# Kernel tuning notes

Measured on AMD Instinct MI355X. Metric: run time of the kernel, lower is better.

The kernel has to match this reference:

```python
import jax, jax.numpy as jnp
import numpy as np

RES = 128
STEPSIZE = 0.5
NEAR, FAR, BG = 0.2, 3.0, 1.0
ALPHA_INIT = 0.01
XYZ_MIN, XYZ_MAX = -1.0, 1.0
N_RAYS = 1024
RGB_LATENT = 15
MULTIRES = 6
EMB_DIM = 3 + 3 * 2 * MULTIRES  # 39
DIM0 = RGB_LATENT + EMB_DIM     # 54
VOXEL = (XYZ_MAX - XYZ_MIN) / RES  # ((2^3)/RES^3)^(1/3)
N_SAMPLES = int(np.linalg.norm(np.array([RES] * 3) * 2 + 1) / STEPSIZE) + 1  # 891
ACT_SHIFT = float(np.log(1.0 / (1.0 - ALPHA_INIT) - 1.0))


def embed_dirs(d):
    # NeRF positional encoding, include_inputs=True, multires=6 -> 39 dims
    freqs = 2.0 ** jnp.arange(MULTIRES, dtype=d.dtype)
    ang = d[..., None, :] * freqs[:, None]  # [M,6,3]
    return jnp.concatenate([d, jnp.sin(ang).reshape(d.shape[0], -1), jnp.cos(ang).reshape(d.shape[0], -1)], -1)


def grid_sample3d(g, coords):
    # g: [C,D,H,W]; coords: [M,3] in (-1,1), torch grid_sample convention
    # (comp0 -> W axis, comp1 -> H axis, comp2 -> D axis), align_corners=True,
    # border-clamped indices (sampled out-of-box points are masked out anyway).
    C, D, H, W = g.shape
    x = (coords[:, 0] + 1) * 0.5 * (W - 1)
    y = (coords[:, 1] + 1) * 0.5 * (H - 1)
    z = (coords[:, 2] + 1) * 0.5 * (D - 1)
    x0, y0, z0 = jnp.floor(x), jnp.floor(y), jnp.floor(z)
    fx, fy, fz = x - x0, y - y0, z - z0
    x0i = jnp.clip(x0.astype(jnp.int32), 0, W - 1); x1i = jnp.clip(x0i + 1, 0, W - 1)
    y0i = jnp.clip(y0.astype(jnp.int32), 0, H - 1); y1i = jnp.clip(y0i + 1, 0, H - 1)
    z0i = jnp.clip(z0.astype(jnp.int32), 0, D - 1); z1i = jnp.clip(z0i + 1, 0, D - 1)
    gf = g.reshape(C, -1)
    def gv(zi, yi, xi):
        return gf[:, (zi * H + yi) * W + xi]  # [C,M]
    c = (((gv(z0i, y0i, x0i) * (1 - fx) + gv(z0i, y0i, x1i) * fx) * (1 - fy)
          + (gv(z0i, y1i, x0i) * (1 - fx) + gv(z0i, y1i, x1i) * fx) * fy) * (1 - fz)
         + ((gv(z1i, y0i, x0i) * (1 - fx) + gv(z1i, y0i, x1i) * fx) * (1 - fy)
            + (gv(z1i, y1i, x0i) * (1 - fx) + gv(z1i, y1i, x1i) * fx) * fy) * fz)
    return c.T  # [M,C]


def _forward(rays_o, rays_d, viewdirs, grid, sobel_kernel, w0, b0, w1, b1, w2, b2, w3, b3):
    # --- sample_ray: ray/AABB intersection + uniform stepping ---
    vec = jnp.where(rays_d == 0, 1e-6, rays_d)
    rate_a = (XYZ_MAX - rays_o) / vec
    rate_b = (XYZ_MIN - rays_o) / vec
    t_min = jnp.clip(jnp.minimum(rate_a, rate_b).max(-1), NEAR, FAR)
    t_max = jnp.clip(jnp.maximum(rate_a, rate_b).min(-1), NEAR, FAR)
    mask_ray = t_max <= t_min
    rng = jnp.arange(N_SAMPLES, dtype=rays_o.dtype)[None]
    step = STEPSIZE * VOXEL * rng
    interpx = t_min[:, None] + step / jnp.linalg.norm(rays_d, axis=-1, keepdims=True)
    pts = rays_o[:, None, :] + rays_d[:, None, :] * interpx[..., None]  # [N,S,3]
    inbox = (~mask_ray[:, None]) & (~((pts < XYZ_MIN) | (pts > XYZ_MAX)).any(-1))
    mflat = inbox.reshape(-1)

    # --- sobel normals grid (GridReg.forward(calc_normals=True)) ---
    density_grid = grid[None, :1]  # [1,1,D,H,W]
    nrm = jax.lax.conv_general_dilated(density_grid, sobel_kernel, (1, 1, 1), [(2, 2)] * 3,
                                       dimension_numbers=('NCDHW', 'OIDHW', 'NCDHW'))  # [1,3,D,H,W]
    nrm = -nrm / jnp.maximum(jnp.linalg.norm(nrm, axis=1, keepdims=True), 1e-12)
    normals_grid = nrm[0]

    # --- extract_latent: trilinear sample at ray points (masked via where) ---
    flat = pts.reshape(-1, 3)
    coords = ((flat - XYZ_MIN) / (XYZ_MAX - XYZ_MIN))[:, ::-1] * 2 - 1  # flip xyz->zyx
    lat = grid_sample3d(grid, coords)          # [M,16]
    ns = grid_sample3d(normals_grid, coords)   # [M,3]
    ns = -ns / jnp.maximum(jnp.linalg.norm(ns, axis=-1, keepdims=True), 1e-12)

    alpha = jnp.where(mflat, 1 - jnp.exp(-jax.nn.softplus(lat[:, 0] + ACT_SHIFT) * STEPSIZE), 0.0)
    alpha = alpha.reshape(N_RAYS, N_SAMPLES)
    normals = jnp.where(mflat[:, None], ns, 0.0).reshape(N_RAYS, N_SAMPLES, 3)
    rgb_lat = jnp.where(mflat[:, None], lat[:, 1:], 0.0)  # [M,15]

    # --- alpha compositing (cumprod_exclusive / get_ray_marching_ray) ---
    alphainv_cum = jnp.concatenate([jnp.ones_like(alpha[:, :1]),
                                    jnp.cumprod(jnp.maximum(1 - alpha, 1e-10), -1)], -1)
    weights = alpha * alphainv_cum[:, :-1]

    # --- reflected-direction shading MLP ---
    v = jnp.broadcast_to(viewdirs[:, None, :], normals.shape)
    dot = jnp.sum(-v * normals, -1, keepdims=True)
    refdirs = (2 * dot * normals + v).reshape(-1, 3)
    feat = jnp.concatenate([rgb_lat, embed_dirs(refdirs)], -1)  # [M,54]
    h = jax.nn.relu(feat @ w0 + b0)
    h = jax.nn.relu(h @ w1 + b1)
    h = jax.nn.relu(h @ w2 + b2)
    col = jax.nn.sigmoid(h @ w3 + b3)
    rgb = jnp.where(mflat[:, None], col, 0.0).reshape(N_RAYS, N_SAMPLES, 3)

    rgb_marched = (weights[..., None] * rgb).sum(-2) + alphainv_cum[:, -1:] * BG
    return rgb_marched


def setup_inputs() -> dict:
    key = jax.random.key(0)
    ks = jax.random.split(key, 8)
    rays_o = 0.3 * jax.random.normal(ks[0], (N_RAYS, 3), jnp.float32)
    rd = jax.random.normal(ks[1], (N_RAYS, 3), jnp.float32)
    rays_d = rd / jnp.linalg.norm(rd, axis=-1, keepdims=True)
    grid = 0.1 * jax.random.normal(ks[2], (1 + RGB_LATENT, RES, RES, RES), jnp.float32)
    sobel_kernel = jax.random.normal(ks[3], (3, 1, 5, 5, 5), jnp.float32)
    def lin(k, i, o):
        return jax.random.normal(k, (i, o), jnp.float32) / np.sqrt(i).astype(np.float32)
    return {
        'rays_o': rays_o, 'rays_d': rays_d, 'viewdirs': rays_d,
        'grid': grid, 'sobel_kernel': sobel_kernel,
        'w0': lin(ks[4], DIM0, 64), 'b0': jnp.zeros((64,), jnp.float32),
        'w1': lin(ks[5], 64, 64), 'b1': jnp.zeros((64,), jnp.float32),
        'w2': lin(ks[6], 64, 64), 'b2': jnp.zeros((64,), jnp.float32),
        'w3': lin(ks[7], 64, 3), 'b3': jnp.zeros((3,), jnp.float32),
    }


def reference(rays_o, rays_d, viewdirs, grid, sobel_kernel, w0, b0, w1, b1, w2, b2, w3, b3):
    return _forward(rays_o, rays_d, viewdirs, grid, sobel_kernel, w0, b0, w1, b1, w2, b2, w3, b3)
```

## Files before the change

### kernel.cpp

```cpp
#include <hip/hip_runtime.h>
#include <hip/hip_bf16.h>
#include <hip/hip_fp16.h>
#include <math.h>

#define RESV 128
#define V3 (RESV*RESV*RESV)
#define N_RAYS 1024
#define N_SAMPLES 891
#define STEP_T 0.0078125f
#define ACT_SHIFT -4.595119850134589f

typedef short bf16x8 __attribute__((ext_vector_type(8)));
typedef float f32x4 __attribute__((ext_vector_type(4)));

__device__ __forceinline__ unsigned short f2b(float x) {
    unsigned int u = __float_as_uint(x);
    unsigned int r = (u + 0x7FFFu + ((u >> 16) & 1u)) >> 16;
    return (unsigned short)r;
}

__device__ __forceinline__ void acc2(float w, unsigned int u, float& lo, float& hi) {
    lo = fmaf(w, __uint_as_float(u << 16), lo);
    hi = fmaf(w, __uint_as_float(u & 0xffff0000u), hi);
}

__global__ __launch_bounds__(256)
void normals_conv_kernel(const float* __restrict__ grid,
                         const float* __restrict__ sobel,
                         float4* __restrict__ nrm4) {
    __shared__ float sk[375];
    const int t = threadIdx.x;
    for (int i = t; i < 375; i += 256) sk[i] = sobel[i];
    __syncthreads();

    const int id = blockIdx.x * 256 + t;
    const int iz4 = (id & 31) * 4;
    const int iy = (id >> 5) & 127;
    const int ix = id >> 12;

    float c0[4] = {0.f, 0.f, 0.f, 0.f};
    float c1[4] = {0.f, 0.f, 0.f, 0.f};
    float c2[4] = {0.f, 0.f, 0.f, 0.f};

    #pragma unroll
    for (int da = -2; da <= 2; ++da) {
        int a = ix + da;
        if ((unsigned)a >= 128u) continue;
        #pragma unroll
        for (int db = -2; db <= 2; ++db) {
            int b = iy + db;
            if ((unsigned)b >= 128u) continue;
            const float* row = grid + (a * 128 + b) * 128;
            const float* k0  = sk + ((da + 2) * 5 + (db + 2)) * 5;
            float g[8];
            #pragma unroll
            for (int m = 0; m < 8; ++m) {
                int c = iz4 - 2 + m;
                int cc = min(max(c, 0), 127);
                float v = row[cc];
                g[m] = ((unsigned)c < 128u) ? v : 0.f;
            }
            #pragma unroll
            for (int zz = 0; zz < 4; ++zz) {
                #pragma unroll
                for (int dc = 0; dc < 5; ++dc) {
                    const float gv = g[zz + dc];
                    c0[zz] = fmaf(gv, k0[dc],       c0[zz]);
                    c1[zz] = fmaf(gv, k0[125 + dc], c1[zz]);
                    c2[zz] = fmaf(gv, k0[250 + dc], c2[zz]);
                }
            }
        }
    }
    const int vbase = (ix * 128 + iy) * 128 + iz4;
    #pragma unroll
    for (int zz = 0; zz < 4; ++zz) {
        float l   = sqrtf(c0[zz]*c0[zz] + c1[zz]*c1[zz] + c2[zz]*c2[zz]);
        float inv = -1.0f / fmaxf(l, 1e-12f);
        nrm4[vbase + zz] = make_float4(c0[zz]*inv, c1[zz]*inv, c2[zz]*inv, 0.f);
    }
}

__global__ __launch_bounds__(256)
void repack_kernel(const float* __restrict__ grid,
                   unsigned short* __restrict__ latp) {
    const int i = blockIdx.x * 256 + threadIdx.x;
    const int v0 = i * 2;
    unsigned int r0[8], r1[8];
    #pragma unroll
    for (int c = 0; c < 16; c += 2) {
        const float2 a = *(const float2*)&grid[(size_t)c * V3 + v0];
        const float2 b = *(const float2*)&grid[(size_t)(c + 1) * V3 + v0];
        r0[c >> 1] = (unsigned int)f2b(a.x) | ((unsigned int)f2b(b.x) << 16);
        r1[c >> 1] = (unsigned int)f2b(a.y) | ((unsigned int)f2b(b.y) << 16);
    }
    uint4* d = (uint4*)&latp[(size_t)v0 * 16];
    d[0] = make_uint4(r0[0], r0[1], r0[2], r0[3]);
    d[1] = make_uint4(r0[4], r0[5], r0[6], r0[7]);
    d[2] = make_uint4(r1[0], r1[1], r1[2], r1[3]);
    d[3] = make_uint4(r1[4], r1[5], r1[6], r1[7]);
}

__device__ __forceinline__ void mfma_layer(unsigned short* __restrict__ actw,
                                           const unsigned short* __restrict__ WT,
                                           const float* __restrict__ Bv,
                                           int r16, int q4, int q8) {
    f32x4 acc[4][4];
    #pragma unroll
    for (int nb = 0; nb < 4; ++nb) {
        const float bv = Bv[nb * 16 + r16];
        #pragma unroll
        for (int mb = 0; mb < 4; ++mb) {
            acc[mb][nb][0] = bv; acc[mb][nb][1] = bv;
            acc[mb][nb][2] = bv; acc[mb][nb][3] = bv;
        }
    }
    #pragma unroll
    for (int ks = 0; ks < 2; ++ks) {
        bf16x8 Af[4], Bf[4];
        #pragma unroll
        for (int mb = 0; mb < 4; ++mb)
            Af[mb] = *(const bf16x8*)&actw[(mb * 16 + r16) * 72 + ks * 32 + q8];
        #pragma unroll
        for (int nb = 0; nb < 4; ++nb)
            Bf[nb] = *(const bf16x8*)&WT[(nb * 16 + r16) * 72 + ks * 32 + q8];
        #pragma unroll
        for (int mb = 0; mb < 4; ++mb) {
            #pragma unroll
            for (int nb = 0; nb < 4; ++nb)
                acc[mb][nb] = __builtin_amdgcn_mfma_f32_16x16x32_bf16(
                    Af[mb], Bf[nb], acc[mb][nb], 0, 0, 0);
        }
    }
    #pragma unroll
    for (int mb = 0; mb < 4; ++mb) {
        #pragma unroll
        for (int nb = 0; nb < 4; ++nb) {
            #pragma unroll
            for (int r = 0; r < 4; ++r) {
                const int row = mb * 16 + q4 + r;
                actw[row * 72 + nb * 16 + r16] = f2b(fmaxf(acc[mb][nb][r], 0.f));
            }
        }
    }
}

#define WT0_OFF 0
#define WT1_OFF (64*72)
#define WT2_OFF (128*72)
#define WT3_OFF (192*72)

template <bool PL>
__global__ __launch_bounds__(256)
void raymarch_kernel(const float* __restrict__ ro, const float* __restrict__ rd,
                     const float* __restrict__ vd, const float* __restrict__ grid,
                     const float4* __restrict__ nrm4,
                     const unsigned short* __restrict__ latp,
                     const float* __restrict__ w0, const float* __restrict__ b0,
                     const float* __restrict__ w1, const float* __restrict__ b1,
                     const float* __restrict__ w2, const float* __restrict__ b2,
                     const float* __restrict__ w3, const float* __restrict__ b3,
                     float* __restrict__ out) {
    __shared__ __align__(16) unsigned short sWT[208 * 72];
    __shared__ __align__(16) unsigned short act[4 * 64 * 72];
    __shared__ float sb0f[64], sb1f[64], sb2f[64], sb3f[16];
    __shared__ __half salpha[1024];
    __shared__ __half scr[1024], scg[1024], scb[1024];
    __shared__ float lgl[1024];
    __shared__ float aux[256];
    __shared__ float red[12];

    const int t = threadIdx.x;
    const int ray = blockIdx.x;
    const int lane = t & 63;
    const int wave = t >> 6;
    const int r16 = lane & 15;
    const int q4 = (lane >> 4) * 4;
    const int q8 = (lane >> 4) * 8;
    unsigned short* const actw = act + wave * 64 * 72;

    for (int i = t; i < 64 * 72; i += 256) {
        int o = i / 72, k = i % 72;
        sWT[WT0_OFF + i] = f2b((k < 54) ? w0[k * 64 + o] : 0.f);
        sWT[WT1_OFF + i] = f2b((k < 64) ? w1[k * 64 + o] : 0.f);
        sWT[WT2_OFF + i] = f2b((k < 64) ? w2[k * 64 + o] : 0.f);
    }
    for (int i = t; i < 16 * 72; i += 256) {
        int n = i / 72, k = i % 72;
        sWT[WT3_OFF + i] = f2b((n < 3 && k < 64) ? w3[k * 3 + n] : 0.f);
    }
    if (t < 64) { sb0f[t] = b0[t]; sb1f[t] = b1[t]; sb2f[t] = b2[t]; }
    if (t < 16) sb3f[t] = (t < 3) ? b3[t] : 0.f;
    __syncthreads();

    const float ox = ro[ray * 3 + 0], oy = ro[ray * 3 + 1], oz = ro[ray * 3 + 2];
    const float dx = rd[ray * 3 + 0], dyv = rd[ray * 3 + 1], dzv = rd[ray * 3 + 2];
    const float vx = vd[ray * 3 + 0], vy = vd[ray * 3 + 1], vz = vd[ray * 3 + 2];

    const float ex = (dx  == 0.f) ? 1e-6f : dx;
    const float ey = (dyv == 0.f) ? 1e-6f : dyv;
    const float ez = (dzv == 0.f) ? 1e-6f : dzv;
    const float rax = (1.f - ox) / ex, rbx = (-1.f - ox) / ex;
    const float ray_ = (1.f - oy) / ey, rby = (-1.f - oy) / ey;
    const float raz = (1.f - oz) / ez, rbz = (-1.f - oz) / ez;
    float tmin = fmaxf(fmaxf(fminf(rax, rbx), fminf(ray_, rby)), fminf(raz, rbz));
    float tmax = fminf(fminf(fmaxf(rax, rbx), fmaxf(ray_, rby)), fmaxf(raz, rbz));
    tmin = fminf(fmaxf(tmin, 0.2f), 3.0f);
    tmax = fminf(fmaxf(tmax, 0.2f), 3.0f);
    const bool mask_ray = (tmax <= tmin);
    const float invn = 1.0f / sqrtf(dx * dx + dyv * dyv + dzv * dzv);

    #pragma unroll 1
    for (int j = 0; j < 4; ++j) {
        const int s = j * 256 + t;
        float alpha_s = 0.f;
        bool active = (s < N_SAMPLES) && !mask_ray;
        float px = 0.f, py = 0.f, pz = 0.f;
        if (active) {
            const float ti = tmin + STEP_T * (float)s * invn;
            px = fmaf(dx, ti, ox);
            py = fmaf(dyv, ti, oy);
            pz = fmaf(dzv, ti, oz);
            active = !(px < -1.f || px > 1.f || py < -1.f || py > 1.f ||
                       pz < -1.f || pz > 1.f);
        }
        const unsigned long long wmask = __ballot(active);
        if (wmask == 0ull) {
            salpha[s] = __float2half(0.f);
            lgl[s] = 0.f;
            scr[s] = __float2half(0.f); scg[s] = __float2half(0.f);
            scb[s] = __float2half(0.f);
            continue;
        }

        float feat[54];
        #pragma unroll
        for (int i = 0; i < 54; ++i) feat[i] = 0.f;

        if (active) {
            const float ga = (px + 1.f) * 63.5f;
            const float gb = (py + 1.f) * 63.5f;
            const float gc = (pz + 1.f) * 63.5f;
            const float fla = floorf(ga), flb = floorf(gb), flc = floorf(gc);
            const float fa = ga - fla, fb = gb - flb, fc = gc - flc;
            int ia0 = min(max((int)fla, 0), 127);
            int ib0 = min(max((int)flb, 0), 127);
            int ic0 = min(max((int)flc, 0), 127);
            int ia1 = min(ia0 + 1, 127);
            int ib1 = min(ib0 + 1, 127);
            int ic1 = min(ic0 + 1, 127);
            const int base00 = (ia0 * 128 + ib0) * 128;
            const int base01 = (ia0 * 128 + ib1) * 128;
            const int base10 = (ia1 * 128 + ib0) * 128;
            const int base11 = (ia1 * 128 + ib1) * 128;
            int idxs[8] = { base00 + ic0, base00 + ic1, base01 + ic0, base01 + ic1,
                            base10 + ic0, base10 + ic1, base11 + ic0, base11 + ic1 };
            const float wa0 = 1.f - fa, wb0 = 1.f - fb, wc0 = 1.f - fc;
            float w8[8] = { wa0*wb0*wc0, wa0*wb0*fc, wa0*fb*wc0, wa0*fb*fc,
                            fa*wb0*wc0,  fa*wb0*fc,  fa*fb*wc0,  fa*fb*fc };

            float lat[16];
            #pragma unroll
            for (int c = 0; c < 16; ++c) lat[c] = 0.f;
            if constexpr (PL) {
                #pragma unroll
                for (int k = 0; k < 8; ++k) {
                    const uint4* rec = (const uint4*)&latp[(size_t)idxs[k] * 16];
                    const uint4 u0 = rec[0];
                    const uint4 u1 = rec[1];
                    const float w = w8[k];
                    acc2(w, u0.x, lat[0],  lat[1]);
                    acc2(w, u0.y, lat[2],  lat[3]);
                    acc2(w, u0.z, lat[4],  lat[5]);
                    acc2(w, u0.w, lat[6],  lat[7]);
                    acc2(w, u1.x, lat[8],  lat[9]);
                    acc2(w, u1.y, lat[10], lat[11]);
                    acc2(w, u1.z, lat[12], lat[13]);
                    acc2(w, u1.w, lat[14], lat[15]);
                }
            } else {
                #pragma unroll
                for (int c = 0; c < 16; ++c) {
                    const float* gcp = grid + (size_t)c * V3;
                    float acc = 0.f;
                    #pragma unroll
                    for (int k = 0; k < 8; ++k) acc = fmaf(w8[k], gcp[idxs[k]], acc);
                    lat[c] = acc;
                }
            }
            const float lat0 = lat[0];
            #pragma unroll
            for (int c = 0; c < 15; ++c) feat[c] = lat[c + 1];

            float n0 = 0.f, n1 = 0.f, n2 = 0.f;
            #pragma unroll
            for (int k = 0; k < 8; ++k) {
                const float4 nv = nrm4[idxs[k]];
                n0 = fmaf(w8[k], nv.x, n0);
                n1 = fmaf(w8[k], nv.y, n1);
                n2 = fmaf(w8[k], nv.z, n2);
            }
            const float nl = sqrtf(n0*n0 + n1*n1 + n2*n2);
            const float ninv = -1.0f / fmaxf(nl, 1e-12f);
            n0 *= ninv; n1 *= ninv; n2 *= ninv;
            const float dotv = -(vx * n0 + vy * n1 + vz * n2);
            const float rx = fmaf(2.f * dotv, n0, vx);
            const float ry = fmaf(2.f * dotv, n1, vy);
            const float rz = fmaf(2.f * dotv, n2, vz);

            const float d0 = lat0 + ACT_SHIFT;
            const float sp = (d0 > 20.f) ? d0 : __logf(1.f + __expf(d0));
            alpha_s = 1.f - __expf(-sp * 0.5f);

            feat[15] = rx; feat[16] = ry; feat[17] = rz;
            float fr = 1.f;
            #pragma unroll
            for (int k = 0; k < 6; ++k) {
                feat[18 + k*3 + 0] = __sinf(rx * fr);
                feat[18 + k*3 + 1] = __sinf(ry * fr);
                feat[18 + k*3 + 2] = __sinf(rz * fr);
                feat[36 + k*3 + 0] = __cosf(rx * fr);
                feat[36 + k*3 + 1] = __cosf(ry * fr);
                feat[36 + k*3 + 2] = __cosf(rz * fr);
                fr *= 2.f;
            }
        }
        salpha[s] = __float2half(alpha_s);
        lgl[s] = __logf(fmaxf(1.f - alpha_s, 1e-10f));

        unsigned int* arow = (unsigned int*)&act[(size_t)t * 72];
        #pragma unroll
        for (int p = 0; p < 27; ++p)
            arow[p] = (unsigned int)f2b(feat[2*p]) |
                      ((unsigned int)f2b(feat[2*p + 1]) << 16);
        #pragma unroll
        for (int p = 27; p < 32; ++p) arow[p] = 0u;

        mfma_layer(actw, sWT + WT0_OFF, sb0f, r16, q4, q8);
        mfma_layer(actw, sWT + WT1_OFF, sb1f, r16, q4, q8);
        mfma_layer(actw, sWT + WT2_OFF, sb2f, r16, q4, q8);

        {
            f32x4 acch[4];
            const float bv = sb3f[r16];
            #pragma unroll
            for (int mb = 0; mb < 4; ++mb) {
                acch[mb][0] = bv; acch[mb][1] = bv;
                acch[mb][2] = bv; acch[mb][3] = bv;
            }
            #pragma unroll
            for (int ks = 0; ks < 2; ++ks) {
                const bf16x8 Bh = *(const bf16x8*)&sWT[WT3_OFF + r16 * 72 + ks * 32 + q8];
                #pragma unroll
                for (int mb = 0; mb < 4; ++mb) {
                    const bf16x8 Af = *(const bf16x8*)&actw[(mb * 16 + r16) * 72 + ks * 32 + q8];
                    acch[mb] = __builtin_amdgcn_mfma_f32_16x16x32_bf16(Af, Bh, acch[mb], 0, 0, 0);
                }
            }
            if (r16 < 3) {
                __half* dst = (r16 == 0) ? scr : (r16 == 1) ? scg : scb;
                const int jb = j * 256 + wave * 64;
                #pragma unroll
                for (int mb = 0; mb < 4; ++mb) {
                    #pragma unroll
                    for (int r = 0; r < 4; ++r) {
                        const int samp = mb * 16 + q4 + r;
                        dst[jb + samp] = __float2half(1.f / (1.f + __expf(-acch[mb][r])));
                    }
                }
            }
        }
    }
    __syncthreads();

    {
        float c0 = lgl[4*t + 0];
        float c1 = c0 + lgl[4*t + 1];
        float c2 = c1 + lgl[4*t + 2];
        float c3 = c2 + lgl[4*t + 3];
        lgl[4*t + 0] = c0; lgl[4*t + 1] = c1;
        lgl[4*t + 2] = c2; lgl[4*t + 3] = c3;
        aux[t] = c3;
    }
    __syncthreads();
    for (int off = 1; off < 256; off <<= 1) {
        const float v = (t >= off) ? aux[t - off] : 0.f;
        __syncthreads();
        aux[t] += v;
        __syncthreads();
    }
    const float total = aux[255];

    float r0 = 0.f, r1 = 0.f, r2 = 0.f;
    #pragma unroll
    for (int j = 0; j < 4; ++j) {
        const int s = j * 256 + t;
        const float a = __half2float(salpha[s]);
        if (s < N_SAMPLES && a > 0.f) {
            float G;
            if (s == 0) G = 0.f;
            else {
                const int m = s - 1;
                G = lgl[m] + (((m >> 2) > 0) ? aux[(m >> 2) - 1] : 0.f);
            }
            const float T = __expf(G);
            const float w = a * T;
            r0 = fmaf(w, __half2float(scr[s]), r0);
            r1 = fmaf(w, __half2float(scg[s]), r1);
            r2 = fmaf(w, __half2float(scb[s]), r2);
        }
    }
    #pragma unroll
    for (int off = 32; off > 0; off >>= 1) {
        r0 += __shfl_down(r0, off, 64);
        r1 += __shfl_down(r1, off, 64);
        r2 += __shfl_down(r2, off, 64);
    }
    if ((t & 63) == 0) {
        red[wave * 3 + 0] = r0; red[wave * 3 + 1] = r1; red[wave * 3 + 2] = r2;
    }
    __syncthreads();
    if (t == 0) {
        const float Tf = __expf(total);
        out[ray * 3 + 0] = red[0] + red[3] + red[6] + red[9]  + Tf;
        out[ray * 3 + 1] = red[1] + red[4] + red[7] + red[10] + Tf;
        out[ray * 3 + 2] = red[2] + red[5] + red[8] + red[11] + Tf;
    }
}

extern "C" void kernel_launch(void* const* d_in, const int* in_sizes, int n_in,
                              void* d_out, int out_size, void* d_ws, size_t ws_size,
                              hipStream_t stream) {
    (void)in_sizes; (void)n_in; (void)out_size;
    const float* ro    = (const float*)d_in[0];
    const float* rd    = (const float*)d_in[1];
    const float* vd    = (const float*)d_in[2];
    const float* grid  = (const float*)d_in[3];
    const float* sobel = (const float*)d_in[4];
    const float* w0 = (const float*)d_in[5];
    const float* b0 = (const float*)d_in[6];
    const float* w1 = (const float*)d_in[7];
    const float* b1 = (const float*)d_in[8];
    const float* w2 = (const float*)d_in[9];
    const float* b2 = (const float*)d_in[10];
    const float* w3 = (const float*)d_in[11];
    const float* b3 = (const float*)d_in[12];

    float4* nrm4 = (float4*)d_ws;
    const size_t NRM_BYTES = (size_t)V3 * 16;
    const size_t LAT_BYTES = (size_t)V3 * 32;
    unsigned short* latp = (unsigned short*)((char*)d_ws + NRM_BYTES);
    const bool packed = (ws_size >= NRM_BYTES + LAT_BYTES);

    normals_conv_kernel<<<V3 / 4 / 256, 256, 0, stream>>>(grid, sobel, nrm4);
    if (packed) {
        repack_kernel<<<V3 / 2 / 256, 256, 0, stream>>>(grid, latp);
        raymarch_kernel<true><<<N_RAYS, 256, 0, stream>>>(ro, rd, vd, grid, nrm4, latp,
                                                          w0, b0, w1, b1, w2, b2, w3, b3,
                                                          (float*)d_out);
    } else {
        raymarch_kernel<false><<<N_RAYS, 256, 0, stream>>>(ro, rd, vd, grid, nrm4, latp,
                                                           w0, b0, w1, b1, w2, b2, w3, b3,
                                                           (float*)d_out);
    }
}
```

Before: 368.1 us.

## Stage Sobel conv halo tile in LDS and widen repack loads to float4

The normals convolution now loads a 5x12 row halo (x by y, full z) of the density grid into shared memory per block, with zero padding, and each thread reads its z window with vectorized LDS loads instead of 25 scattered global row reads. This is meant to cut redundant global and L2 traffic for the 5x5x5 stencil. The repack kernel now handles four voxels per thread with float4 loads. The trade-off is about 32KB of LDS per block, which may lower occupancy.

New measurement: 344.5 us. -6.4%, faster.

```diff
diff --git a/kernel.cpp b/kernel.cpp
--- a/kernel.cpp
+++ b/kernel.cpp
@@ -24,47 +24,64 @@
     hi = fmaf(w, __uint_as_float(u & 0xffff0000u), hi);
 }
 
+#define ROWS 60
+#define ZSTR 136
+
 __global__ __launch_bounds__(256)
 void normals_conv_kernel(const float* __restrict__ grid,
                          const float* __restrict__ sobel,
                          float4* __restrict__ nrm4) {
     __shared__ float sk[375];
+    __shared__ __align__(16) float tile[ROWS * ZSTR];
+
     const int t = threadIdx.x;
+    const int bx = blockIdx.x;
+    const int ix = bx >> 4;
+    const int iy0 = (bx & 15) * 8;
+
     for (int i = t; i < 375; i += 256) sk[i] = sobel[i];
+
+    {
+        const int lane32 = t & 31;
+        for (int r = t >> 5; r < ROWS; r += 8) {
+            const int xl = r / 12, yl = r % 12;
+            const int gx = ix + xl - 2;
+            const int gy = iy0 + yl - 2;
+            float4 v = make_float4(0.f, 0.f, 0.f, 0.f);
+            if ((unsigned)gx < 128u && (unsigned)gy < 128u)
+                v = *(const float4*)&grid[(size_t)(gx * 128 + gy) * 128 + lane32 * 4];
+            *(float4*)&tile[r * ZSTR + 4 + lane32 * 4] = v;
+        }
+        if (t < ROWS) {
+            float* row = tile + t * ZSTR;
+            row[0] = 0.f; row[1] = 0.f; row[2] = 0.f; row[3] = 0.f;
+            row[132] = 0.f; row[133] = 0.f; row[134] = 0.f; row[135] = 0.f;
+        }
+    }
     __syncthreads();
 
-    const int id = blockIdx.x * 256 + t;
-    const int iz4 = (id & 31) * 4;
-    const int iy = (id >> 5) & 127;
-    const int ix = id >> 12;
+    const int iz4 = (t & 31) * 4;
+    const int iyl = t >> 5;
 
     float c0[4] = {0.f, 0.f, 0.f, 0.f};
     float c1[4] = {0.f, 0.f, 0.f, 0.f};
     float c2[4] = {0.f, 0.f, 0.f, 0.f};
 
     #pragma unroll
-    for (int da = -2; da <= 2; ++da) {
-        int a = ix + da;
-        if ((unsigned)a >= 128u) continue;
-        #pragma unroll
-        for (int db = -2; db <= 2; ++db) {
-            int b = iy + db;
-            if ((unsigned)b >= 128u) continue;
-            const float* row = grid + (a * 128 + b) * 128;
-            const float* k0  = sk + ((da + 2) * 5 + (db + 2)) * 5;
-            float g[8];
-            #pragma unroll
-            for (int m = 0; m < 8; ++m) {
-                int c = iz4 - 2 + m;
-                int cc = min(max(c, 0), 127);
-                float v = row[cc];
-                g[m] = ((unsigned)c < 128u) ? v : 0.f;
-            }
+    for (int da = 0; da < 5; ++da) {
+        #pragma unroll
+        for (int db = 0; db < 5; ++db) {
+            const float* row = tile + (da * 12 + iyl + db + 2) * ZSTR;
+            const float* k0  = sk + (da * 5 + db) * 5;
+            float gbuf[12];
+            *(float4*)&gbuf[0] = *(const float4*)&row[iz4];
+            *(float4*)&gbuf[4] = *(const float4*)&row[iz4 + 4];
+            *(float4*)&gbuf[8] = *(const float4*)&row[iz4 + 8];
             #pragma unroll
             for (int zz = 0; zz < 4; ++zz) {
                 #pragma unroll
                 for (int dc = 0; dc < 5; ++dc) {
-                    const float gv = g[zz + dc];
+                    const float gv = gbuf[2 + zz + dc];
                     c0[zz] = fmaf(gv, k0[dc],       c0[zz]);
                     c1[zz] = fmaf(gv, k0[125 + dc], c1[zz]);
                     c2[zz] = fmaf(gv, k0[250 + dc], c2[zz]);
@@ -72,7 +89,7 @@
             }
         }
     }
-    const int vbase = (ix * 128 + iy) * 128 + iz4;
+    const int vbase = (ix * 128 + iy0 + iyl) * 128 + iz4;
     #pragma unroll
     for (int zz = 0; zz < 4; ++zz) {
         float l   = sqrtf(c0[zz]*c0[zz] + c1[zz]*c1[zz] + c2[zz]*c2[zz]);
@@ -85,20 +102,23 @@
 void repack_kernel(const float* __restrict__ grid,
                    unsigned short* __restrict__ latp) {
     const int i = blockIdx.x * 256 + threadIdx.x;
-    const int v0 = i * 2;
-    unsigned int r0[8], r1[8];
+    const int v0 = i * 4;
+    unsigned int r[4][8];
     #pragma unroll
     for (int c = 0; c < 16; c += 2) {
-        const float2 a = *(const float2*)&grid[(size_t)c * V3 + v0];
-        const float2 b = *(const float2*)&grid[(size_t)(c + 1) * V3 + v0];
-        r0[c >> 1] = (unsigned int)f2b(a.x) | ((unsigned int)f2b(b.x) << 16);
-        r1[c >> 1] = (unsigned int)f2b(a.y) | ((unsigned int)f2b(b.y) << 16);
+        const float4 a = *(const float4*)&grid[(size_t)c * V3 + v0];
+        const float4 b = *(const float4*)&grid[(size_t)(c + 1) * V3 + v0];
+        const float* pa = &a.x; const float* pb = &b.x;
+        #pragma unroll
+        for (int z = 0; z < 4; ++z)
+            r[z][c >> 1] = (unsigned int)f2b(pa[z]) | ((unsigned int)f2b(pb[z]) << 16);
     }
     uint4* d = (uint4*)&latp[(size_t)v0 * 16];
-    d[0] = make_uint4(r0[0], r0[1], r0[2], r0[3]);
-    d[1] = make_uint4(r0[4], r0[5], r0[6], r0[7]);
-    d[2] = make_uint4(r1[0], r1[1], r1[2], r1[3]);
-    d[3] = make_uint4(r1[4], r1[5], r1[6], r1[7]);
+    #pragma unroll
+    for (int z = 0; z < 4; ++z) {
+        d[z * 2 + 0] = make_uint4(r[z][0], r[z][1], r[z][2], r[z][3]);
+        d[z * 2 + 1] = make_uint4(r[z][4], r[z][5], r[z][6], r[z][7]);
+    }
 }
 
 __device__ __forceinline__ void mfma_layer(unsigned short* __restrict__ actw,
@@ -452,9 +472,9 @@
     unsigned short* latp = (unsigned short*)((char*)d_ws + NRM_BYTES);
     const bool packed = (ws_size >= NRM_BYTES + LAT_BYTES);
 
-    normals_conv_kernel<<<V3 / 4 / 256, 256, 0, stream>>>(grid, sobel, nrm4);
+    normals_conv_kernel<<<128 * 16, 256, 0, stream>>>(grid, sobel, nrm4);
     if (packed) {
-        repack_kernel<<<V3 / 2 / 256, 256, 0, stream>>>(grid, latp);
+        repack_kernel<<<V3 / 4 / 256, 256, 0, stream>>>(grid, latp);
         raymarch_kernel<true><<<N_RAYS, 256, 0, stream>>>(ro, rd, vd, grid, nrm4, latp,
                                                           w0, b0, w1, b1, w2, b2, w3, b3,
                                                           (float*)d_out);
```
